# Kernel tuning notes

Measured on AMD Instinct MI355X. Metric: run time of the kernel, lower is better.

The kernel has to match this reference:

```python
import jax, jax.numpy as jnp
import numpy as np

N_AGENTS = 5
RNN = 128
ATT = 64
N_ACT = 10
IN_DIM = 256
SIZE = 65535  # multiple of N_AGENTS -> padding branch never taken
TAU = 0.01


def _gru_cell(x, h, w_ih, w_hh, b_ih, b_hh):
    # PyTorch GRUCell math
    gi = x @ w_ih.T + b_ih
    gh = h @ w_hh.T + b_hh
    i_r, i_z, i_n = jnp.split(gi, 3, axis=-1)
    h_r, h_z, h_n = jnp.split(gh, 3, axis=-1)
    r = jax.nn.sigmoid(i_r + h_r)
    z = jax.nn.sigmoid(i_z + h_z)
    n = jnp.tanh(i_n + r * h_n)
    return (1.0 - z) * n + z * h


def _gru_seq(xs, w_ih, w_hh, b_ih, b_hh):
    # xs: [T, B, D]; zero initial hidden, returns all step outputs [T, B, RNN]
    h0 = jnp.zeros((xs.shape[1], RNN), xs.dtype)
    def step(h, x):
        h2 = _gru_cell(x, h, w_ih, w_hh, b_ih, b_hh)
        return h2, h2
    _, ys = jax.lax.scan(step, h0, xs)
    return ys


def setup_inputs():
    key = jax.random.key(0)
    ks = jax.random.split(key, 26)
    def u(k, shape, fan):
        return jax.random.uniform(k, shape, jnp.float32, -1.0, 1.0) / np.sqrt(fan)
    return {
        'obs': jax.random.normal(ks[0], (SIZE, IN_DIM), jnp.float32),
        'hidden_state': jax.random.normal(ks[1], (SIZE, RNN), jnp.float32),
        'enc_w': u(ks[2], (RNN, IN_DIM), IN_DIM), 'enc_b': u(ks[3], (RNN,), IN_DIM),
        'gru_w_ih': u(ks[4], (3 * RNN, RNN), RNN), 'gru_w_hh': u(ks[5], (3 * RNN, RNN), RNN),
        'gru_b_ih': u(ks[6], (3 * RNN,), RNN), 'gru_b_hh': u(ks[7], (3 * RNN,), RNN),
        'bi_w_ih_f': u(ks[8], (3 * RNN, 2 * RNN), RNN), 'bi_w_hh_f': u(ks[9], (3 * RNN, RNN), RNN),
        'bi_b_ih_f': u(ks[10], (3 * RNN,), RNN), 'bi_b_hh_f': u(ks[11], (3 * RNN,), RNN),
        'bi_w_ih_r': u(ks[12], (3 * RNN, 2 * RNN), RNN), 'bi_w_hh_r': u(ks[13], (3 * RNN, RNN), RNN),
        'bi_b_ih_r': u(ks[14], (3 * RNN,), RNN), 'bi_b_hh_r': u(ks[15], (3 * RNN,), RNN),
        'hard_w': u(ks[16], (2, 2 * RNN), 2 * RNN), 'hard_b': u(ks[17], (2,), 2 * RNN),
        'q_w': u(ks[18], (ATT, RNN), RNN),
        'k_w': u(ks[19], (ATT, RNN), RNN),
        'v_w': u(ks[20], (ATT, RNN), RNN), 'v_b': u(ks[21], (ATT,), RNN),
        'dec_w': u(ks[22], (N_ACT, RNN + ATT), RNN + ATT), 'dec_b': u(ks[23], (N_ACT,), RNN + ATT),
    }


def reference(obs, hidden_state, enc_w, enc_b, gru_w_ih, gru_w_hh, gru_b_ih, gru_b_hh,
              bi_w_ih_f, bi_w_hh_f, bi_b_ih_f, bi_b_hh_f,
              bi_w_ih_r, bi_w_hh_r, bi_b_ih_r, bi_b_hh_r,
              hard_w, hard_b, q_w, k_w, v_w, v_b, dec_w, dec_b):
    size = obs.shape[0]
    bpa = size // N_AGENTS  # batch per agent; SIZE is a multiple of N_AGENTS

    x = jax.nn.relu(obs @ enc_w.T + enc_b)
    h_out = _gru_cell(x, hidden_state, gru_w_ih, gru_w_hh, gru_b_ih, gru_b_hh)

    # --- hard attention: pairwise agent features -> bi-GRU -> gumbel-softmax gate ---
    # (computed exactly as in the original; note the original soft_attention
    #  ignores hard_weights, so this does not influence the returned output)
    h = h_out.reshape(bpa, N_AGENTS, RNN)
    nbr = np.array([[j for j in range(N_AGENTS) if j != i] for i in range(N_AGENTS)])  # [n, n-1]
    h_i = jnp.broadcast_to(h[:, :, None, :], (bpa, N_AGENTS, N_AGENTS - 1, RNN))
    h_j = h[:, nbr, :]                              # [bpa, n, n-1, RNN]
    pair = jnp.concatenate([h_i, h_j], axis=-1)     # [bpa, n, n-1, 2*RNN]
    seq = pair.transpose(2, 0, 1, 3).reshape(N_AGENTS - 1, bpa * N_AGENTS, 2 * RNN)
    fwd = _gru_seq(seq, bi_w_ih_f, bi_w_hh_f, bi_b_ih_f, bi_b_hh_f)
    bwd = _gru_seq(seq[::-1], bi_w_ih_r, bi_w_hh_r, bi_b_ih_r, bi_b_hh_r)[::-1]
    h_hard = jnp.concatenate([fwd, bwd], axis=-1)   # [n-1, B, 2*RNN]
    h_hard = h_hard.transpose(1, 0, 2).reshape(-1, 2 * RNN)
    logits = h_hard @ hard_w.T + hard_b             # [B*(n-1), 2]
    u01 = jax.random.uniform(jax.random.key(42), logits.shape, jnp.float32, 1e-10, 1.0)
    gumbel = -jnp.log(-jnp.log(u01))
    gs = jax.nn.softmax((logits + gumbel) / TAU, axis=-1)
    hard_weights = gs[:, 1].reshape(bpa, N_AGENTS, 1, N_AGENTS - 1).transpose(1, 0, 2, 3)
    _ = hard_weights  # unused downstream, matching the original module

    # --- soft attention: original loops per sample doing a 1x1 matmul+softmax;
    #     vectorized here. softmax over a single element is identically 1. ---
    q = h_out @ q_w.T
    k = h_out @ k_w.T
    v = jax.nn.relu(h_out @ v_w.T + v_b)
    score = jnp.sum(q * k, axis=-1, keepdims=True) / np.sqrt(ATT)  # [B,1]
    soft_w = jax.nn.softmax(score, axis=-1)                         # all ones
    x_att = v * soft_w

    final_input = jnp.concatenate([h_out, x_att], axis=-1)
    output = final_input @ dec_w.T + dec_b
    return output, h_out
```

## Files before the change

### kernel.cpp

```cpp
#include <hip/hip_runtime.h>
#include <stdint.h>

#define SIZE 65535

typedef __bf16 bf16x8 __attribute__((ext_vector_type(8)));
typedef float floatx4 __attribute__((ext_vector_type(4)));

#define WS_ENCW 0
#define WS_WIH  32768
#define WS_WHH  81920
#define WS_VW   131072
#define WS_DECW 139264
#define WS_TOTC 17792

__device__ __forceinline__ unsigned short f2bf(float f) {
    union { float f; unsigned int u; } v; v.f = f;
    unsigned int u = v.u;
    return (unsigned short)((u + 0x7fffu + ((u >> 16) & 1u)) >> 16);
}
__device__ __forceinline__ unsigned short f2bfn(float f) {
    union { __bf16 h; unsigned short s; } u; u.h = (__bf16)f;
    return u.s;
}
__device__ __forceinline__ float bf2f(unsigned short b) {
    union { unsigned int u; float f; } v; v.u = ((unsigned int)b) << 16;
    return v.f;
}
__device__ __forceinline__ float sigmf(float x) {
    x = fminf(fmaxf(x, -30.f), 30.f);
    return 1.f / (1.f + __expf(-x));
}
__device__ __forceinline__ float tanhfast(float x) {
    x = fminf(fmaxf(x, -15.f), 15.f);
    float e = __expf(2.f * x);
    return (e - 1.f) / (e + 1.f);
}

__device__ __forceinline__ bf16x8 cvt8g(const float* p) {
    float4 a = *reinterpret_cast<const float4*>(p);
    float4 b = *reinterpret_cast<const float4*>(p + 4);
    bf16x8 r;
    r[0] = (__bf16)a.x; r[1] = (__bf16)a.y; r[2] = (__bf16)a.z; r[3] = (__bf16)a.w;
    r[4] = (__bf16)b.x; r[5] = (__bf16)b.y; r[6] = (__bf16)b.z; r[7] = (__bf16)b.w;
    return r;
}
__device__ __forceinline__ bf16x8 ld8(const unsigned short* p) {
    return *reinterpret_cast<const bf16x8*>(p);
}

__device__ __forceinline__ void glds16(const unsigned short* g, unsigned short* l) {
    __builtin_amdgcn_global_load_lds(
        (const __attribute__((address_space(1))) unsigned int*)g,
        (__attribute__((address_space(3))) unsigned int*)l, 16, 0, 0);
}

__device__ __forceinline__ void stage_seq(unsigned short* dst, const unsigned short* src,
                                          int nfrags, int wave, int lane) {
    for (int s = wave; s < nfrags; s += 4)
        glds16(src + s * 512 + lane * 8, dst + s * 512);
}
__device__ __forceinline__ void stage_gru(unsigned short* dst, const unsigned short* wsw,
                                          int ng, int wave, int lane) {
    const int fo = (ng * 4 + wave) * 512 + lane * 8;
    glds16(wsw + WS_WIH + fo, dst + wave * 512);
    glds16(wsw + WS_WHH + fo, dst + (4 + wave) * 512);
}

__global__ __launch_bounds__(256) void cvt_weights(
    const float* __restrict__ enc_w, const float* __restrict__ w_ih,
    const float* __restrict__ w_hh, const float* __restrict__ v_w,
    const float* __restrict__ dec_w, unsigned short* __restrict__ ws) {
    int c = blockIdx.x * 256 + threadIdx.x;
    if (c >= WS_TOTC) return;
    const int lane = c & 63;
    const int l = lane & 15;
    const int q = lane >> 4;
    const float* src; int row, col, stride; bool zero = false;
    if (c < 4096) {
        int lt = c >> 6; int nt = lt >> 3, kt = lt & 7;
        row = nt * 16 + l; col = kt * 32 + q * 8; src = enc_w; stride = 256;
    } else if (c < 10240) {
        int lt = (c - 4096) >> 6; int nt = lt / 12; int r2 = lt % 12;
        int g = r2 >> 2, kt = r2 & 3;
        row = g * 128 + nt * 16 + l; col = kt * 32 + q * 8; src = w_ih; stride = 128;
    } else if (c < 16384) {
        int lt = (c - 10240) >> 6; int nt = lt / 12; int r2 = lt % 12;
        int g = r2 >> 2, kt = r2 & 3;
        row = g * 128 + nt * 16 + l; col = kt * 32 + q * 8; src = w_hh; stride = 128;
    } else if (c < 17408) {
        int lt = (c - 16384) >> 6; int nt = lt >> 2, kt = lt & 3;
        row = nt * 16 + l; col = kt * 32 + q * 8; src = v_w; stride = 128;
    } else {
        int kt = (c - 17408) >> 6;
        row = l; col = kt * 32 + q * 8; src = dec_w; stride = 192;
        zero = (l >= 10);
    }
    float4 a, b;
    if (zero) { a = make_float4(0.f,0.f,0.f,0.f); b = a; }
    else {
        const float* p = src + (size_t)row * stride + col;
        a = *reinterpret_cast<const float4*>(p);
        b = *reinterpret_cast<const float4*>(p + 4);
    }
    unsigned short* d = ws + (size_t)c * 8;
    d[0]=f2bf(a.x); d[1]=f2bf(a.y); d[2]=f2bf(a.z); d[3]=f2bf(a.w);
    d[4]=f2bf(b.x); d[5]=f2bf(b.y); d[6]=f2bf(b.z); d[7]=f2bf(b.w);
}

__global__ __launch_bounds__(256, 4) void attn_critic_kernel(
    const float* __restrict__ obs,
    const float* __restrict__ hid,
    const float* __restrict__ enc_b,
    const float* __restrict__ b_ih,
    const float* __restrict__ b_hh,
    const float* __restrict__ v_b,
    const float* __restrict__ dec_b,
    const unsigned short* __restrict__ wsw,
    float* __restrict__ out)
{
    __shared__ __align__(16) unsigned short wbuf[2][4096];
    __shared__ __align__(16) unsigned short pool[4][2176];

    const int tid  = threadIdx.x;
    const int wave = tid >> 6;
    const int lane = tid & 63;
    const int l15  = lane & 15;
    const int quad = lane >> 4;
    const int wrow0 = (blockIdx.x * 4 + wave) * 16;

    unsigned short (*sA)[136] = (unsigned short(*)[136])&pool[wave][0];
    unsigned short (*sV)[72]  = (unsigned short(*)[72]) &pool[wave][0];
    float* sO = (float*)&pool[wave][1152];

    int rA0 = wrow0 + l15; rA0 = (rA0 < SIZE) ? rA0 : (SIZE - 1);

    stage_seq(wbuf[0], wsw + WS_ENCW, 8, wave, lane);

    bf16x8 aob[8], hf[4];
    {
        const float* o0 = obs + (size_t)rA0 * 256;
#pragma unroll
        for (int kt = 0; kt < 8; ++kt)
            aob[kt] = cvt8g(o0 + kt * 32 + quad * 8);
        const float* h0 = hid + (size_t)rA0 * 128;
#pragma unroll
        for (int kt = 0; kt < 4; ++kt)
            hf[kt] = cvt8g(h0 + kt * 32 + quad * 8);
    }
    __builtin_amdgcn_sched_barrier(0);
    __syncthreads();

#pragma unroll 1
    for (int nt = 0; nt < 8; ++nt) {
        const int cur = nt & 1;
        if (nt < 7) stage_seq(wbuf[cur ^ 1], wsw + WS_ENCW + (nt + 1) * 4096, 8, wave, lane);
        else        stage_gru(wbuf[cur ^ 1], wsw, 0, wave, lane);
        const float bias = enc_b[nt * 16 + l15];
        floatx4 a0 = floatx4{0.f,0.f,0.f,0.f};
#pragma unroll
        for (int kt = 0; kt < 8; ++kt) {
            bf16x8 b = ld8(&wbuf[cur][kt * 512 + lane * 8]);
            a0 = __builtin_amdgcn_mfma_f32_16x16x32_bf16(aob[kt], b, a0, 0, 0, 0);
        }
#pragma unroll
        for (int r = 0; r < 4; ++r)
            sA[quad * 4 + r][nt * 16 + l15] = f2bfn(fmaxf(a0[r] + bias, 0.f));
        __syncthreads();
    }

    bf16x8 xf[4];
#pragma unroll
    for (int kt = 0; kt < 4; ++kt)
        xf[kt] = ld8(&sA[l15][kt * 32 + quad * 8]);

#pragma unroll 1
    for (int nt = 0; nt < 8; ++nt) {
        const int nr = nt * 16 + l15;
        float hp[4];
#pragma unroll
        for (int r = 0; r < 4; ++r) {
            const int grow = wrow0 + quad * 4 + r;
            const int rowc = (grow < SIZE) ? grow : (SIZE - 1);
            hp[r] = hid[(size_t)rowc * 128 + nr];
        }
        const float bir_ = b_ih[nr], biz_ = b_ih[nr + 128], bin_ = b_ih[nr + 256];
        const float bhr_ = b_hh[nr], bhz_ = b_hh[nr + 128], bhn_ = b_hh[nr + 256];
        floatx4 gi[3], gh[3];
#pragma unroll
        for (int g = 0; g < 3; ++g) {
            gi[g] = floatx4{0.f,0.f,0.f,0.f};
            gh[g] = gi[g];
        }
#pragma unroll
        for (int g = 0; g < 3; ++g) {
            const int cur = (nt + g) & 1;
            const int ng = nt * 3 + g + 1;
            if (ng < 24) stage_gru(wbuf[cur ^ 1], wsw, ng, wave, lane);
            else         stage_seq(wbuf[cur ^ 1], wsw + WS_VW, 4, wave, lane);
#pragma unroll
            for (int kt = 0; kt < 4; ++kt) {
                bf16x8 bi = ld8(&wbuf[cur][kt * 512 + lane * 8]);
                bf16x8 bh = ld8(&wbuf[cur][(4 + kt) * 512 + lane * 8]);
                gi[g] = __builtin_amdgcn_mfma_f32_16x16x32_bf16(xf[kt], bi, gi[g], 0, 0, 0);
                gh[g] = __builtin_amdgcn_mfma_f32_16x16x32_bf16(hf[kt], bh, gh[g], 0, 0, 0);
            }
            __syncthreads();
        }
#pragma unroll
        for (int r = 0; r < 4; ++r) {
            float rg = sigmf(gi[0][r] + bir_ + gh[0][r] + bhr_);
            float zg = sigmf(gi[1][r] + biz_ + gh[1][r] + bhz_);
            float ng2 = tanhfast(gi[2][r] + bin_ + rg * (gh[2][r] + bhn_));
            float ho = (1.f - zg) * ng2 + zg * hp[r];
            sA[quad * 4 + r][nr] = f2bfn(ho);
        }
    }

    bf16x8 af[4];
#pragma unroll
    for (int kt = 0; kt < 4; ++kt)
        af[kt] = ld8(&sA[l15][kt * 32 + quad * 8]);
    {
        float* out_h = out + (size_t)SIZE * 10;
#pragma unroll 1
        for (int it = 0; it < 8; ++it) {
            int idx = it * 256 + lane * 4;
            int rr = idx >> 7, cc = idx & 127;
            int grow = wrow0 + rr;
            if (grow < SIZE) {
                float2 p0 = make_float2(bf2f(sA[rr][cc]),     bf2f(sA[rr][cc + 1]));
                float2 p1 = make_float2(bf2f(sA[rr][cc + 2]), bf2f(sA[rr][cc + 3]));
                float* dst = out_h + (size_t)grow * 128 + cc;
                *reinterpret_cast<float2*>(dst)     = p0;
                *reinterpret_cast<float2*>(dst + 2) = p1;
            }
        }
    }

#pragma unroll 1
    for (int nt = 0; nt < 4; ++nt) {
        const int cur = nt & 1;
        if (nt < 3) stage_seq(wbuf[cur ^ 1], wsw + WS_VW + (nt + 1) * 2048, 4, wave, lane);
        else        stage_seq(wbuf[cur ^ 1], wsw + WS_DECW, 6, wave, lane);
        const float bias = v_b[nt * 16 + l15];
        floatx4 a0 = floatx4{0.f,0.f,0.f,0.f};
#pragma unroll
        for (int kt = 0; kt < 4; ++kt) {
            bf16x8 b = ld8(&wbuf[cur][kt * 512 + lane * 8]);
            a0 = __builtin_amdgcn_mfma_f32_16x16x32_bf16(af[kt], b, a0, 0, 0, 0);
        }
#pragma unroll
        for (int r = 0; r < 4; ++r)
            sV[quad * 4 + r][nt * 16 + l15] = f2bfn(fmaxf(a0[r] + bias, 0.f));
        __syncthreads();
    }

    {
        floatx4 d0 = floatx4{0.f,0.f,0.f,0.f};
#pragma unroll
        for (int kt = 0; kt < 6; ++kt) {
            bf16x8 b = ld8(&wbuf[0][kt * 512 + lane * 8]);
            bf16x8 a0 = (kt < 4) ? af[kt] : ld8(&sV[l15][(kt - 4) * 32 + quad * 8]);
            d0 = __builtin_amdgcn_mfma_f32_16x16x32_bf16(a0, b, d0, 0, 0, 0);
        }
        if (l15 < 10) {
            const float bias = dec_b[l15];
#pragma unroll
            for (int r = 0; r < 4; ++r)
                sO[(quad * 4 + r) * 10 + l15] = d0[r] + bias;
        }
#pragma unroll
        for (int j = 0; j < 3; ++j) {
            int idx = j * 64 + lane;
            if (idx < 160) {
                int row = idx / 10, col = idx % 10;
                int grow = wrow0 + row;
                if (grow < SIZE)
                    out[(size_t)grow * 10 + col] = sO[row * 10 + col];
            }
        }
    }
}

extern "C" void kernel_launch(void* const* d_in, const int* in_sizes, int n_in,
                              void* d_out, int out_size, void* d_ws, size_t ws_size,
                              hipStream_t stream) {
    const float* obs   = (const float*)d_in[0];
    const float* hid   = (const float*)d_in[1];
    const float* enc_w = (const float*)d_in[2];
    const float* enc_b = (const float*)d_in[3];
    const float* w_ih  = (const float*)d_in[4];
    const float* w_hh  = (const float*)d_in[5];
    const float* b_ih  = (const float*)d_in[6];
    const float* b_hh  = (const float*)d_in[7];
    const float* v_w   = (const float*)d_in[20];
    const float* v_b   = (const float*)d_in[21];
    const float* dec_w = (const float*)d_in[22];
    const float* dec_b = (const float*)d_in[23];
    unsigned short* wsw = (unsigned short*)d_ws;
    float* out = (float*)d_out;

    hipLaunchKernelGGL(cvt_weights, dim3((WS_TOTC + 255) / 256), dim3(256), 0, stream,
                       enc_w, w_ih, w_hh, v_w, dec_w, wsw);
    hipLaunchKernelGGL(attn_critic_kernel, dim3(1024), dim3(256), 0, stream,
                       obs, hid, enc_b, b_ih, b_hh, v_b, dec_b, wsw, out);
}
```

Before: 208.5 us.

## Stage weights in large LDS chunks with 512-thread blocks and fewer barriers

```diff
diff --git a/kernel.cpp b/kernel.cpp
--- a/kernel.cpp
+++ b/kernel.cpp
@@ -52,18 +52,6 @@
     __builtin_amdgcn_global_load_lds(
         (const __attribute__((address_space(1))) unsigned int*)g,
         (__attribute__((address_space(3))) unsigned int*)l, 16, 0, 0);
-}
-
-__device__ __forceinline__ void stage_seq(unsigned short* dst, const unsigned short* src,
-                                          int nfrags, int wave, int lane) {
-    for (int s = wave; s < nfrags; s += 4)
-        glds16(src + s * 512 + lane * 8, dst + s * 512);
-}
-__device__ __forceinline__ void stage_gru(unsigned short* dst, const unsigned short* wsw,
-                                          int ng, int wave, int lane) {
-    const int fo = (ng * 4 + wave) * 512 + lane * 8;
-    glds16(wsw + WS_WIH + fo, dst + wave * 512);
-    glds16(wsw + WS_WHH + fo, dst + (4 + wave) * 512);
 }
 
 __global__ __launch_bounds__(256) void cvt_weights(
@@ -107,7 +95,7 @@
     d[4]=f2bf(b.x); d[5]=f2bf(b.y); d[6]=f2bf(b.z); d[7]=f2bf(b.w);
 }
 
-__global__ __launch_bounds__(256, 4) void attn_critic_kernel(
+__global__ __launch_bounds__(512) void attn_critic_kernel(
     const float* __restrict__ obs,
     const float* __restrict__ hid,
     const float* __restrict__ enc_b,
@@ -118,15 +106,15 @@
     const unsigned short* __restrict__ wsw,
     float* __restrict__ out)
 {
-    __shared__ __align__(16) unsigned short wbuf[2][4096];
-    __shared__ __align__(16) unsigned short pool[4][2176];
+    __shared__ __align__(16) unsigned short wA[49152];
+    __shared__ __align__(16) unsigned short pool[8][2176];
 
     const int tid  = threadIdx.x;
     const int wave = tid >> 6;
     const int lane = tid & 63;
     const int l15  = lane & 15;
     const int quad = lane >> 4;
-    const int wrow0 = (blockIdx.x * 4 + wave) * 16;
+    const int wrow0 = (blockIdx.x * 8 + wave) * 16;
 
     unsigned short (*sA)[136] = (unsigned short(*)[136])&pool[wave][0];
     unsigned short (*sV)[72]  = (unsigned short(*)[72]) &pool[wave][0];
@@ -134,7 +122,9 @@
 
     int rA0 = wrow0 + l15; rA0 = (rA0 < SIZE) ? rA0 : (SIZE - 1);
 
-    stage_seq(wbuf[0], wsw + WS_ENCW, 8, wave, lane);
+#pragma unroll
+    for (int i = 0; i < 8; ++i)
+        glds16(wsw + WS_ENCW + i * 4096 + tid * 8, wA + i * 4096 + tid * 8);
 
     bf16x8 aob[8], hf[4];
     {
@@ -152,69 +142,89 @@
 
 #pragma unroll 1
     for (int nt = 0; nt < 8; ++nt) {
-        const int cur = nt & 1;
-        if (nt < 7) stage_seq(wbuf[cur ^ 1], wsw + WS_ENCW + (nt + 1) * 4096, 8, wave, lane);
-        else        stage_gru(wbuf[cur ^ 1], wsw, 0, wave, lane);
         const float bias = enc_b[nt * 16 + l15];
         floatx4 a0 = floatx4{0.f,0.f,0.f,0.f};
 #pragma unroll
         for (int kt = 0; kt < 8; ++kt) {
-            bf16x8 b = ld8(&wbuf[cur][kt * 512 + lane * 8]);
+            bf16x8 b = ld8(&wA[(nt * 8 + kt) * 512 + lane * 8]);
             a0 = __builtin_amdgcn_mfma_f32_16x16x32_bf16(aob[kt], b, a0, 0, 0, 0);
         }
 #pragma unroll
         for (int r = 0; r < 4; ++r)
             sA[quad * 4 + r][nt * 16 + l15] = f2bfn(fmaxf(a0[r] + bias, 0.f));
-        __syncthreads();
     }
 
     bf16x8 xf[4];
 #pragma unroll
     for (int kt = 0; kt < 4; ++kt)
         xf[kt] = ld8(&sA[l15][kt * 32 + quad * 8]);
-
+    __syncthreads();
+
+    auto gru_quarter = [&](int h4) {
 #pragma unroll 1
-    for (int nt = 0; nt < 8; ++nt) {
-        const int nr = nt * 16 + l15;
-        float hp[4];
-#pragma unroll
-        for (int r = 0; r < 4; ++r) {
-            const int grow = wrow0 + quad * 4 + r;
-            const int rowc = (grow < SIZE) ? grow : (SIZE - 1);
-            hp[r] = hid[(size_t)rowc * 128 + nr];
-        }
-        const float bir_ = b_ih[nr], biz_ = b_ih[nr + 128], bin_ = b_ih[nr + 256];
-        const float bhr_ = b_hh[nr], bhz_ = b_hh[nr + 128], bhn_ = b_hh[nr + 256];
-        floatx4 gi[3], gh[3];
-#pragma unroll
-        for (int g = 0; g < 3; ++g) {
-            gi[g] = floatx4{0.f,0.f,0.f,0.f};
-            gh[g] = gi[g];
-        }
-#pragma unroll
-        for (int g = 0; g < 3; ++g) {
-            const int cur = (nt + g) & 1;
-            const int ng = nt * 3 + g + 1;
-            if (ng < 24) stage_gru(wbuf[cur ^ 1], wsw, ng, wave, lane);
-            else         stage_seq(wbuf[cur ^ 1], wsw + WS_VW, 4, wave, lane);
-#pragma unroll
-            for (int kt = 0; kt < 4; ++kt) {
-                bf16x8 bi = ld8(&wbuf[cur][kt * 512 + lane * 8]);
-                bf16x8 bh = ld8(&wbuf[cur][(4 + kt) * 512 + lane * 8]);
-                gi[g] = __builtin_amdgcn_mfma_f32_16x16x32_bf16(xf[kt], bi, gi[g], 0, 0, 0);
-                gh[g] = __builtin_amdgcn_mfma_f32_16x16x32_bf16(hf[kt], bh, gh[g], 0, 0, 0);
-            }
-            __syncthreads();
-        }
-#pragma unroll
-        for (int r = 0; r < 4; ++r) {
-            float rg = sigmf(gi[0][r] + bir_ + gh[0][r] + bhr_);
-            float zg = sigmf(gi[1][r] + biz_ + gh[1][r] + bhz_);
-            float ng2 = tanhfast(gi[2][r] + bin_ + rg * (gh[2][r] + bhn_));
-            float ho = (1.f - zg) * ng2 + zg * hp[r];
-            sA[quad * 4 + r][nr] = f2bfn(ho);
-        }
-    }
+        for (int ntL = 0; ntL < 4; ++ntL) {
+            const int nt = h4 + ntL;
+            const int nr = nt * 16 + l15;
+            float hp[4];
+#pragma unroll
+            for (int r = 0; r < 4; ++r) {
+                const int grow = wrow0 + quad * 4 + r;
+                const int rowc = (grow < SIZE) ? grow : (SIZE - 1);
+                hp[r] = hid[(size_t)rowc * 128 + nr];
+            }
+            const float bir_ = b_ih[nr], biz_ = b_ih[nr + 128], bin_ = b_ih[nr + 256];
+            const float bhr_ = b_hh[nr], bhz_ = b_hh[nr + 128], bhn_ = b_hh[nr + 256];
+            floatx4 gi[3], gh[3];
+#pragma unroll
+            for (int g = 0; g < 3; ++g) {
+                gi[g] = floatx4{0.f,0.f,0.f,0.f};
+                gh[g] = gi[g];
+            }
+#pragma unroll
+            for (int g = 0; g < 3; ++g)
+#pragma unroll
+                for (int kt = 0; kt < 4; ++kt) {
+                    bf16x8 bi = ld8(&wA[((ntL * 3 + g) * 4 + kt) * 512 + lane * 8]);
+                    bf16x8 bh = ld8(&wA[24576 + ((ntL * 3 + g) * 4 + kt) * 512 + lane * 8]);
+                    gi[g] = __builtin_amdgcn_mfma_f32_16x16x32_bf16(xf[kt], bi, gi[g], 0, 0, 0);
+                    gh[g] = __builtin_amdgcn_mfma_f32_16x16x32_bf16(hf[kt], bh, gh[g], 0, 0, 0);
+                }
+#pragma unroll
+            for (int r = 0; r < 4; ++r) {
+                float rg = sigmf(gi[0][r] + bir_ + gh[0][r] + bhr_);
+                float zg = sigmf(gi[1][r] + biz_ + gh[1][r] + bhz_);
+                float ng2 = tanhfast(gi[2][r] + bin_ + rg * (gh[2][r] + bhn_));
+                float ho = (1.f - zg) * ng2 + zg * hp[r];
+                sA[quad * 4 + r][nr] = f2bfn(ho);
+            }
+        }
+    };
+
+#pragma unroll
+    for (int i = 0; i < 6; ++i) {
+        const int o = i * 4096 + tid * 8;
+        glds16(wsw + WS_WIH + o, wA + o);
+        glds16(wsw + WS_WHH + o, wA + 24576 + o);
+    }
+    __syncthreads();
+    gru_quarter(0);
+    __syncthreads();
+
+#pragma unroll
+    for (int i = 0; i < 6; ++i) {
+        const int o = i * 4096 + tid * 8;
+        glds16(wsw + WS_WIH + 24576 + o, wA + o);
+        glds16(wsw + WS_WHH + 24576 + o, wA + 24576 + o);
+    }
+    __syncthreads();
+    gru_quarter(4);
+    __syncthreads();
+
+#pragma unroll
+    for (int i = 0; i < 2; ++i)
+        glds16(wsw + WS_VW + i * 4096 + tid * 8, wA + i * 4096 + tid * 8);
+    if (tid < 384)
+        glds16(wsw + WS_DECW + tid * 8, wA + 8192 + tid * 8);
 
     bf16x8 af[4];
 #pragma unroll
@@ -236,30 +246,27 @@
             }
         }
     }
+    __syncthreads();
 
 #pragma unroll 1
     for (int nt = 0; nt < 4; ++nt) {
-        const int cur = nt & 1;
-        if (nt < 3) stage_seq(wbuf[cur ^ 1], wsw + WS_VW + (nt + 1) * 2048, 4, wave, lane);
-        else        stage_seq(wbuf[cur ^ 1], wsw + WS_DECW, 6, wave, lane);
         const float bias = v_b[nt * 16 + l15];
         floatx4 a0 = floatx4{0.f,0.f,0.f,0.f};
 #pragma unroll
         for (int kt = 0; kt < 4; ++kt) {
-            bf16x8 b = ld8(&wbuf[cur][kt * 512 + lane * 8]);
+            bf16x8 b = ld8(&wA[(nt * 4 + kt) * 512 + lane * 8]);
             a0 = __builtin_amdgcn_mfma_f32_16x16x32_bf16(af[kt], b, a0, 0, 0, 0);
         }
 #pragma unroll
         for (int r = 0; r < 4; ++r)
             sV[quad * 4 + r][nt * 16 + l15] = f2bfn(fmaxf(a0[r] + bias, 0.f));
-        __syncthreads();
     }
 
     {
         floatx4 d0 = floatx4{0.f,0.f,0.f,0.f};
 #pragma unroll
         for (int kt = 0; kt < 6; ++kt) {
-            bf16x8 b = ld8(&wbuf[0][kt * 512 + lane * 8]);
+            bf16x8 b = ld8(&wA[8192 + kt * 512 + lane * 8]);
             bf16x8 a0 = (kt < 4) ? af[kt] : ld8(&sV[l15][(kt - 4) * 32 + quad * 8]);
             d0 = __builtin_amdgcn_mfma_f32_16x16x32_bf16(a0, b, d0, 0, 0, 0);
         }
@@ -302,6 +309,6 @@
 
     hipLaunchKernelGGL(cvt_weights, dim3((WS_TOTC + 255) / 256), dim3(256), 0, stream,
                        enc_w, w_ih, w_hh, v_w, dec_w, wsw);
-    hipLaunchKernelGGL(attn_critic_kernel, dim3(1024), dim3(256), 0, stream,
+    hipLaunchKernelGGL(attn_critic_kernel, dim3(512), dim3(512), 0, stream,
                        obs, hid, enc_b, b_ih, b_hh, v_b, dec_b, wsw, out);
 }
```

After: 213.0 us. 2.2% more time.
